# Optimization experiments

Hardware: AMD Instinct MI355X
Metric: run time of the kernel (lower is better)

The kernel has to match this reference:

```python
import jax, jax.numpy as jnp
import numpy as np

EMBED = 1024

def setup_inputs() -> dict:
    key = jax.random.key(0)
    kx, kq, kk, kv = jax.random.split(key, 4)
    x = jax.random.normal(kx, (4, 2048, EMBED), dtype=jnp.float32)
    s = 1.0 / np.sqrt(EMBED)
    Wq = jax.random.normal(kq, (EMBED, EMBED), dtype=jnp.float32) * s
    Wk = jax.random.normal(kk, (EMBED, EMBED), dtype=jnp.float32) * s
    Wv = jax.random.normal(kv, (EMBED, EMBED), dtype=jnp.float32) * s
    return {"x": x, "Wq": Wq, "Wk": Wk, "Wv": Wv}

def reference(x, Wq, Wk, Wv):
    # x: [b, s, e]; nn.Linear(y) = y @ W.T, weights stored [out, in]
    Q = jnp.einsum('bse,oe->bso', x, Wq)
    K = jnp.einsum('bse,oe->bso', x, Wk)
    V = jnp.einsum('bse,oe->bso', x, Wv)
    scale = 1.0 / jnp.sqrt(jnp.asarray(x.shape[-1], x.dtype))
    energy = jnp.einsum('bqe,bke->bqk', Q, K) * scale  # [b, s, s]
    attention = jax.nn.softmax(energy, axis=-1)
    out = jnp.einsum('bqk,bke->bqe', attention, V)
    return out
```

## Files before the change

kernel.cpp:

```cpp
#include <hip/hip_runtime.h>
#include <stdint.h>


typedef __attribute__((ext_vector_type(8))) short bf16x8;
typedef __attribute__((ext_vector_type(4))) float f32x4;

__device__ __forceinline__ float bf2f(uint16_t u) {
    return __uint_as_float(((uint32_t)u) << 16);
}
__device__ __forceinline__ uint16_t f2bf(float f) {
    uint32_t u = __float_as_uint(f);
    uint32_t r = u + 0x7FFFu + ((u >> 16) & 1u);
    return (uint16_t)(r >> 16);
}

__device__ __forceinline__ void gll16(const void* g, void* l) {
    __builtin_amdgcn_global_load_lds(
        (const __attribute__((address_space(1))) uint32_t*)g,
        (__attribute__((address_space(3))) uint32_t*)l,
        16, 0, 0);
}

template <int NC>
__device__ __forceinline__ void stageT(const uint16_t* g, long stride,
                                       uint16_t* l, int tid) {
    #pragma unroll
    for (int c = 0; c < NC; ++c)
        gll16(g + (long)c * 64 * stride, l + c * 4096 + tid * 8);
}

__global__ __launch_bounds__(256) void cast_all(const float* __restrict__ x,
                                                const float* __restrict__ Wq,
                                                const float* __restrict__ Wk,
                                                const float* __restrict__ Wv,
                                                uint16_t* __restrict__ xb,
                                                uint16_t* __restrict__ wqkvb,
                                                int NX4, int NW4) {
    int i = blockIdx.x * 256 + threadIdx.x;
    const float* src;
    uint16_t* dst;
    int off;
    if (i < NX4) {
        src = x; dst = xb; off = i;
    } else {
        int j = i - NX4;
        if (j >= 3 * NW4) return;
        int which = j / NW4;
        off = j - which * NW4;
        src = (which == 0) ? Wq : (which == 1) ? Wk : Wv;
        dst = wqkvb + (size_t)which * NW4 * 4;
    }
    float4 v = ((const float4*)src)[off];
    ushort4 o;
    o.x = f2bf(v.x); o.y = f2bf(v.y); o.z = f2bf(v.z); o.w = f2bf(v.w);
    ((ushort4*)dst)[off] = o;
}

__global__ __launch_bounds__(256) void softmax_rows(uint16_t* __restrict__ P) {
    const int n = 2048;
    uint16_t* row = P + (size_t)blockIdx.x * n;
    int tid = threadIdx.x;
    int w = tid >> 6, ln = tid & 63;
    float v[8];
    float m = -3.4e38f;
    #pragma unroll
    for (int i = 0; i < 8; i++) { v[i] = bf2f(row[tid + 256 * i]); m = fmaxf(m, v[i]); }
    #pragma unroll
    for (int o = 32; o >= 1; o >>= 1) m = fmaxf(m, __shfl_down(m, o, 64));
    __shared__ float smax[4], ssum[4];
    if (ln == 0) smax[w] = m;
    __syncthreads();
    m = fmaxf(fmaxf(smax[0], smax[1]), fmaxf(smax[2], smax[3]));
    float s = 0.f;
    #pragma unroll
    for (int i = 0; i < 8; i++) { v[i] = __expf(v[i] - m); s += v[i]; }
    #pragma unroll
    for (int o = 32; o >= 1; o >>= 1) s += __shfl_down(s, o, 64);
    if (ln == 0) ssum[w] = s;
    __syncthreads();
    s = ssum[0] + ssum[1] + ssum[2] + ssum[3];
    float inv = 1.f / s;
    #pragma unroll
    for (int i = 0; i < 8; i++) row[tid + 256 * i] = f2bf(v[i] * inv);
}


#define DS_A(mh_) do { \
    _Pragma("unroll") for (int f_ = 0; f_ < MH; ++f_) { \
        const uint16_t* p_ = Asb + axbase + ((mh_)*MH + f_) * 1024; \
        af[f_][0] = *(const bf16x8*)(p_ + cs0); \
        af[f_][1] = *(const bf16x8*)(p_ + cs1); \
    } } while (0)

#define DS_B(nh_) do { \
    _Pragma("unroll") for (int n_ = 0; n_ < 2; ++n_) { \
        const uint16_t* p_ = Bsb + bxbase + ((nh_)*2 + n_) * 1024; \
        bf[nh_][n_][0] = *(const bf16x8*)(p_ + cs0); \
        bf[nh_][n_][1] = *(const bf16x8*)(p_ + cs1); \
    } } while (0)

#define MMA(mh_, nh_) do { \
    _Pragma("unroll") for (int f_ = 0; f_ < MH; ++f_) { \
        _Pragma("unroll") for (int n_ = 0; n_ < 2; ++n_) { \
            acc[(mh_)*MH + f_][(nh_)*2 + n_] = __builtin_amdgcn_mfma_f32_16x16x32_bf16( \
                af[f_][0], bf[nh_][n_][0], acc[(mh_)*MH + f_][(nh_)*2 + n_], 0, 0, 0); \
            acc[(mh_)*MH + f_][(nh_)*2 + n_] = __builtin_amdgcn_mfma_f32_16x16x32_bf16( \
                af[f_][1], bf[nh_][n_][1], acc[(mh_)*MH + f_][(nh_)*2 + n_], 0, 0, 0); \
        } } } while (0)

#define PH_ENTER do { \
    asm volatile("s_barrier\n\ts_waitcnt lgkmcnt(0)" ::: "memory"); \
    __builtin_amdgcn_s_setprio(1); } while (0)

#define PH_EXIT do { \
    __builtin_amdgcn_s_setprio(0); \
    asm volatile("s_barrier" ::: "memory"); } while (0)

template <int BM, typename OutT>
__global__ __launch_bounds__(512, 2) void gemm_nt(const uint16_t* __restrict__ A,
                                                  const uint16_t* __restrict__ B,
                                                  OutT* __restrict__ C,
                                                  int gx, int gy,
                                                  long lda, long ldb, long ldc,
                                                  int K, float alpha,
                                                  long sA, long sB, long sC,
                                                  uint16_t* __restrict__ VtP,
                                                  int vcol0) {
    constexpr int MF  = BM / 32;
    constexpr int MH  = MF / 2;
    constexpr int NAC = BM / 64;

    const int total = gridDim.x;
    const int nb  = blockIdx.x;
    const int per = total >> 3;
    const int g   = (nb & 7) * per + (nb >> 3);
    const int pb  = gx * gy;
    const int bz  = g / pb;
    const int r   = g - bz * pb;
    const int stpr = gx >> 2;
    const int st  = r >> 4;
    const int w   = r & 15;
    const int sty = st / stpr;
    const int stx = st - sty * stpr;
    const int bx  = (stx << 2) + (w & 3);
    const int by  = (sty << 2) + (w >> 2);

    A += (long)bz * sA;
    B += (long)bz * sB;
    C += (long)bz * sC;

    __shared__ uint16_t As[2][BM * 64];
    __shared__ uint16_t Bs[2][256 * 64];

    const int tid = threadIdx.x;
    const int m0 = by * BM;
    const int n0 = bx * 256;

    const int srow = tid >> 3;
    const int sx   = ((tid & 7) ^ (srow & 7)) << 3;
    const uint16_t* Ag = A + (long)(m0 + srow) * lda + sx;
    const uint16_t* Bg = B + (long)(n0 + srow) * ldb + sx;

    const int wave = tid >> 6, lane = tid & 63;
    const int quad = lane >> 4, l16 = lane & 15;
    const int wm = wave >> 2, wn = wave & 3;
    const int cs0 = ((quad       ^ (l16 & 7)) << 3);
    const int cs1 = (((quad + 4) ^ (l16 & 7)) << 3);
    const int axbase = (wm * (BM / 2) + l16) * 64;
    const int bxbase = (wn * 64 + l16) * 64;

    const int nk = K / 64;

    f32x4 acc[MF][4] = {};
    bf16x8 af[MH][2];
    bf16x8 bf[2][2][2];

    stageT<NAC>(Ag, lda, &As[0][0], tid);
    stageT<4>(Bg, ldb, &Bs[0][0], tid);
    asm volatile("s_waitcnt vmcnt(0)" ::: "memory");
    asm volatile("s_barrier" ::: "memory");

    for (int kt = 0; kt < nk; ++kt) {
        const int cur = kt & 1, nxt = cur ^ 1;
        const uint16_t* Asb = &As[cur][0];
        const uint16_t* Bsb = &Bs[cur][0];
        const bool pf = (kt + 1 < nk);
        const long ko = (long)(kt + 1) * 64;

        DS_A(0); DS_B(0);
        if (pf) stageT<NAC>(Ag + ko, lda, &As[nxt][0], tid);
        PH_ENTER; MMA(0, 0); PH_EXIT;

        DS_B(1);
        if (pf) stageT<4>(Bg + ko, ldb, &Bs[nxt][0], tid);
        PH_ENTER; MMA(0, 1); PH_EXIT;

        DS_A(1);
        PH_ENTER; MMA(1, 0); PH_EXIT;

        PH_ENTER; MMA(1, 1);
        __builtin_amdgcn_s_setprio(0);
        asm volatile("s_waitcnt vmcnt(0)\n\ts_barrier" ::: "memory");
    }

    if (VtP && n0 >= vcol0) {
        #pragma unroll
        for (int f = 0; f < MF; ++f) {
            const int row0 = m0 + wm * (BM / 2) + f * 16 + quad * 4;
            const int b_   = row0 >> 11;
            const int s_   = row0 & 2047;
            #pragma unroll
            for (int j = 0; j < 4; ++j) {
                const int e = n0 + wn * 64 + j * 16 + l16 - vcol0;
                ushort4 o;
                o.x = f2bf(acc[f][j][0]);
                o.y = f2bf(acc[f][j][1]);
                o.z = f2bf(acc[f][j][2]);
                o.w = f2bf(acc[f][j][3]);
                *(ushort4*)(VtP + ((long)b_ * 1024 + e) * 2048 + s_) = o;
            }
        }
    } else {
        #pragma unroll
        for (int f = 0; f < MF; ++f) {
            #pragma unroll
            for (int j = 0; j < 4; ++j) {
                #pragma unroll
                for (int r4 = 0; r4 < 4; ++r4) {
                    const int row = m0 + wm * (BM / 2) + f * 16 + quad * 4 + r4;
                    const int col = n0 + wn * 64 + j * 16 + l16;
                    const float val = acc[f][j][r4] * alpha;
                    if constexpr (sizeof(OutT) == 2)
                        C[(long)row * ldc + col] = f2bf(val);
                    else
                        C[(long)row * ldc + col] = val;
                }
            }
        }
    }
}

extern "C" void kernel_launch(void* const* d_in, const int* in_sizes, int n_in,
                              void* d_out, int out_size, void* d_ws, size_t ws_size,
                              hipStream_t stream) {
    const float* x  = (const float*)d_in[0];
    const float* Wq = (const float*)d_in[1];
    const float* Wk = (const float*)d_in[2];
    const float* Wv = (const float*)d_in[3];
    float* out = (float*)d_out;

    const int Bn = 4, S = 2048, E = 1024;
    const long MS = (long)Bn * S;
    const int  N3 = 3 * E;

    char* ws = (char*)d_ws;
    uint16_t* xb    = (uint16_t*)ws;  ws += (size_t)MS * E * 2;
    uint16_t* wqkvb = (uint16_t*)ws;  ws += (size_t)N3 * E * 2;
    uint16_t* QKb   = (uint16_t*)ws;  ws += (size_t)MS * 2048 * 2;
    uint16_t* Vt    = (uint16_t*)ws;  ws += (size_t)Bn * E * S * 2;
    uint16_t* Pb    = (uint16_t*)ws;  ws += (size_t)Bn * S * S * 2;

    {
        int NX4 = (int)(MS * E / 4);
        int NW4 = E * E / 4;
        int tot = NX4 + 3 * NW4;
        cast_all<<<dim3((tot + 255) / 256), dim3(256), 0, stream>>>(
            x, Wq, Wk, Wv, xb, wqkvb, NX4, NW4);
    }

    {
        int gx = N3 / 256, gy = (int)(MS / 256);
        gemm_nt<256, uint16_t><<<dim3(gx * gy), dim3(512), 0, stream>>>(
            xb, wqkvb, QKb, gx, gy, E, E, 2048, E, 1.f, 0, 0, 0,
            Vt, 2048);
    }

    {
        int gx = S / 256, gy = S / 256;
        gemm_nt<256, uint16_t><<<dim3(gx * gy * Bn), dim3(512), 0, stream>>>(
            QKb, QKb + 1024, Pb, gx, gy, 2048, 2048, S, E, 0.03125f,
            (long)S * 2048, (long)S * 2048, (long)S * S,
            nullptr, 0);
    }

    softmax_rows<<<dim3(Bn * S), dim3(256), 0, stream>>>(Pb);

    {
        int gx = E / 256, gy = S / 128;
        gemm_nt<128, float><<<dim3(gx * gy * Bn), dim3(512), 0, stream>>>(
            Pb, Vt, out, gx, gy, S, S, E, S, 1.f,
            (long)S * S, (long)E * S, (long)S * E,
            nullptr, 0);
    }
}
```

Baseline: 255.6 us.

## Deepen GEMM prefetch to two tiles ahead with fine-grained vmcnt waits

Restructures the GEMM main loop so global-to-LDS loads are issued two k-tiles ahead into the buffer just consumed, split into per-chunk loads interleaved between MFMA phases. Partial s_waitcnt vmcnt counts replace the full drain at each iteration, and explicit epilogue tiles handle the tail. The QKV projection GEMM also switches from BM=256 to BM=128 tiles, giving more blocks. The goal is to hide memory latency better, at the cost of tricky barrier and count reasoning and possible LDS write-after-read hazards.

```diff
diff --git a/kernel.cpp b/kernel.cpp
--- a/kernel.cpp
+++ b/kernel.cpp
@@ -19,14 +19,6 @@
         (const __attribute__((address_space(1))) uint32_t*)g,
         (__attribute__((address_space(3))) uint32_t*)l,
         16, 0, 0);
-}
-
-template <int NC>
-__device__ __forceinline__ void stageT(const uint16_t* g, long stride,
-                                       uint16_t* l, int tid) {
-    #pragma unroll
-    for (int c = 0; c < NC; ++c)
-        gll16(g + (long)c * 64 * stride, l + c * 4096 + tid * 8);
 }
 
 __global__ __launch_bounds__(256) void cast_all(const float* __restrict__ x,
@@ -95,17 +87,17 @@
 #define DS_B(nh_) do { \
     _Pragma("unroll") for (int n_ = 0; n_ < 2; ++n_) { \
         const uint16_t* p_ = Bsb + bxbase + ((nh_)*2 + n_) * 1024; \
-        bf[nh_][n_][0] = *(const bf16x8*)(p_ + cs0); \
-        bf[nh_][n_][1] = *(const bf16x8*)(p_ + cs1); \
+        bfr[nh_][n_][0] = *(const bf16x8*)(p_ + cs0); \
+        bfr[nh_][n_][1] = *(const bf16x8*)(p_ + cs1); \
     } } while (0)
 
 #define MMA(mh_, nh_) do { \
     _Pragma("unroll") for (int f_ = 0; f_ < MH; ++f_) { \
         _Pragma("unroll") for (int n_ = 0; n_ < 2; ++n_) { \
             acc[(mh_)*MH + f_][(nh_)*2 + n_] = __builtin_amdgcn_mfma_f32_16x16x32_bf16( \
-                af[f_][0], bf[nh_][n_][0], acc[(mh_)*MH + f_][(nh_)*2 + n_], 0, 0, 0); \
+                af[f_][0], bfr[nh_][n_][0], acc[(mh_)*MH + f_][(nh_)*2 + n_], 0, 0, 0); \
             acc[(mh_)*MH + f_][(nh_)*2 + n_] = __builtin_amdgcn_mfma_f32_16x16x32_bf16( \
-                af[f_][1], bf[nh_][n_][1], acc[(mh_)*MH + f_][(nh_)*2 + n_], 0, 0, 0); \
+                af[f_][1], bfr[nh_][n_][1], acc[(mh_)*MH + f_][(nh_)*2 + n_], 0, 0, 0); \
         } } } while (0)
 
 #define PH_ENTER do { \
@@ -115,6 +107,32 @@
 #define PH_EXIT do { \
     __builtin_amdgcn_s_setprio(0); \
     asm volatile("s_barrier" ::: "memory"); } while (0)
+
+#define VMB(n) asm volatile("s_waitcnt vmcnt(" #n ")\n\ts_barrier" ::: "memory")
+#define BARO   asm volatile("s_barrier" ::: "memory")
+#define NOBAR  ((void)0)
+
+#define KTILE(ISSUE, W1B, W3B) do { \
+    const uint16_t* Asb = &As[cur][0]; \
+    const uint16_t* Bsb = &Bs[cur][0]; \
+     \
+    DS_A(0); DS_B(0); \
+    PH_ENTER; MMA(0, 0); PH_EXIT; \
+     \
+    DS_B(1); \
+    if constexpr (BM == 256) { if (ISSUE) { stA(cur, ko2, 0); stA(cur, ko2, 2); } } \
+    PH_ENTER; MMA(0, 1); __builtin_amdgcn_s_setprio(0); W1B; \
+     \
+    DS_A(1); \
+    if (ISSUE) { stB(cur, ko2, 0); stB(cur, ko2, 1); stB(cur, ko2, 2); stB(cur, ko2, 3); } \
+    PH_ENTER; MMA(1, 0); PH_EXIT; \
+     \
+    if (ISSUE) { \
+        if constexpr (BM == 256) { stA(cur, ko2, 1); stA(cur, ko2, 3); } \
+        else                     { stA(cur, ko2, 0); stA(cur, ko2, 1); } \
+    } \
+    PH_ENTER; MMA(1, 1); __builtin_amdgcn_s_setprio(0); W3B; \
+} while (0)
 
 template <int BM, typename OutT>
 __global__ __launch_bounds__(512, 2) void gemm_nt(const uint16_t* __restrict__ A,
@@ -126,9 +144,8 @@
                                                   long sA, long sB, long sC,
                                                   uint16_t* __restrict__ VtP,
                                                   int vcol0) {
-    constexpr int MF  = BM / 32;
-    constexpr int MH  = MF / 2;
-    constexpr int NAC = BM / 64;
+    constexpr int MF = BM / 32;
+    constexpr int MH = MF / 2;
 
     const int total = gridDim.x;
     const int nb  = blockIdx.x;
@@ -161,6 +178,13 @@
     const uint16_t* Ag = A + (long)(m0 + srow) * lda + sx;
     const uint16_t* Bg = B + (long)(n0 + srow) * ldb + sx;
 
+    auto stA = [&](int buf, long ko, int c) {
+        gll16(Ag + (long)c * 64 * lda + ko, &As[buf][c * 4096] + tid * 8);
+    };
+    auto stB = [&](int buf, long ko, int c) {
+        gll16(Bg + (long)c * 64 * ldb + ko, &Bs[buf][c * 4096] + tid * 8);
+    };
+
     const int wave = tid >> 6, lane = tid & 63;
     const int quad = lane >> 4, l16 = lane & 15;
     const int wm = wave >> 2, wn = wave & 3;
@@ -173,34 +197,41 @@
 
     f32x4 acc[MF][4] = {};
     bf16x8 af[MH][2];
-    bf16x8 bf[2][2][2];
-
-    stageT<NAC>(Ag, lda, &As[0][0], tid);
-    stageT<4>(Bg, ldb, &Bs[0][0], tid);
-    asm volatile("s_waitcnt vmcnt(0)" ::: "memory");
-    asm volatile("s_barrier" ::: "memory");
-
-    for (int kt = 0; kt < nk; ++kt) {
-        const int cur = kt & 1, nxt = cur ^ 1;
-        const uint16_t* Asb = &As[cur][0];
-        const uint16_t* Bsb = &Bs[cur][0];
-        const bool pf = (kt + 1 < nk);
-        const long ko = (long)(kt + 1) * 64;
-
-        DS_A(0); DS_B(0);
-        if (pf) stageT<NAC>(Ag + ko, lda, &As[nxt][0], tid);
-        PH_ENTER; MMA(0, 0); PH_EXIT;
-
-        DS_B(1);
-        if (pf) stageT<4>(Bg + ko, ldb, &Bs[nxt][0], tid);
-        PH_ENTER; MMA(0, 1); PH_EXIT;
-
-        DS_A(1);
-        PH_ENTER; MMA(1, 0); PH_EXIT;
-
-        PH_ENTER; MMA(1, 1);
-        __builtin_amdgcn_s_setprio(0);
-        asm volatile("s_waitcnt vmcnt(0)\n\ts_barrier" ::: "memory");
+    bf16x8 bfr[2][2][2];
+
+    if constexpr (BM == 256) {
+        stA(0, 0, 0);  stA(0, 0, 2);
+        stB(0, 0, 0);  stB(0, 0, 1);  stB(0, 0, 2);  stB(0, 0, 3);
+        stA(0, 0, 1);  stA(0, 0, 3);
+        stA(1, 64, 0); stA(1, 64, 2);
+        stB(1, 64, 0); stB(1, 64, 1); stB(1, 64, 2); stB(1, 64, 3);
+        stA(1, 64, 1); stA(1, 64, 3);
+        VMB(10);
+    } else {
+        stB(0, 0, 0);  stB(0, 0, 1);  stB(0, 0, 2);  stB(0, 0, 3);
+        stA(0, 0, 0);  stA(0, 0, 1);
+        stB(1, 64, 0); stB(1, 64, 1); stB(1, 64, 2); stB(1, 64, 3);
+        stA(1, 64, 0); stA(1, 64, 1);
+        VMB(6);
+    }
+
+    int cur = 0;
+    for (int kt = 0; kt < nk - 2; ++kt) {
+        const long ko2 = (long)(kt + 2) * 64;
+        if constexpr (BM == 256) { KTILE(1, VMB(10), VMB(10)); }
+        else                     { KTILE(1, BARO,    VMB(6));  }
+        cur ^= 1;
+    }
+    {
+        const long ko2 = 0; (void)ko2;
+        if constexpr (BM == 256) { KTILE(0, VMB(8), VMB(2)); }
+        else                     { KTILE(0, BARO,   VMB(0)); }
+        cur ^= 1;
+    }
+    {
+        const long ko2 = 0; (void)ko2;
+        if constexpr (BM == 256) { KTILE(0, VMB(0), NOBAR); }
+        else                     { KTILE(0, BARO,   NOBAR); }
     }
 
     if (VtP && n0 >= vcol0) {
@@ -269,8 +300,8 @@
     }
 
     {
-        int gx = N3 / 256, gy = (int)(MS / 256);
-        gemm_nt<256, uint16_t><<<dim3(gx * gy), dim3(512), 0, stream>>>(
+        int gx = N3 / 256, gy = (int)(MS / 128);
+        gemm_nt<128, uint16_t><<<dim3(gx * gy), dim3(512), 0, stream>>>(
             xb, wqkvb, QKb, gx, gy, E, E, 2048, E, 1.f, 0, 0, 0,
             Vt, 2048);
     }
```

Result: no change. 252.8 us (-1.1%).
